# Kernel tuning notes

Hardware: AMD Instinct MI355X
Metric: run time of the kernel (lower is better)

The kernel has to match this reference:

```python
import jax, jax.numpy as jnp
import numpy as np

N_NODES = 50000
N_EDGES = 800000
N_GRAPHS = 512
HIDDEN = 256
NODE_FEAT = 9
LAYERS = 4


def setup_inputs() -> dict:
    key = jax.random.key(0)
    ks = jax.random.split(key, 9)
    x = jax.random.normal(ks[0], (N_NODES, NODE_FEAT), dtype=jnp.float32)
    edge_index = jax.random.randint(ks[1], (2, N_EDGES), 0, N_NODES, dtype=jnp.int64)
    batch = jnp.sort(jax.random.randint(ks[2], (N_NODES,), 0, N_GRAPHS, dtype=jnp.int64))
    embed_W = jax.random.normal(ks[3], (NODE_FEAT, HIDDEN), dtype=jnp.float32) * (1.0 / np.sqrt(NODE_FEAT))
    embed_b = jnp.zeros((HIDDEN,), dtype=jnp.float32)
    conv_W = jax.random.normal(ks[4], (LAYERS, HIDDEN, HIDDEN), dtype=jnp.float32) * (1.0 / np.sqrt(HIDDEN))
    conv_b = jnp.zeros((LAYERS, HIDDEN), dtype=jnp.float32)
    out_W = jax.random.normal(ks[5], (HIDDEN, 1), dtype=jnp.float32) * (1.0 / np.sqrt(HIDDEN))
    out_b = jnp.zeros((1,), dtype=jnp.float32)
    return {"x": x, "edge_index": edge_index, "batch": batch,
            "embed_W": embed_W, "embed_b": embed_b,
            "conv_W": conv_W, "conv_b": conv_b,
            "out_W": out_W, "out_b": out_b}


def reference(x, edge_index, batch, embed_W, embed_b, conv_W, conv_b, out_W, out_b):
    n = x.shape[0]
    src, dst = edge_index[0], edge_index[1]
    # GCN symmetric normalization with self-loops: deg includes the self-loop (+1)
    deg = jax.ops.segment_sum(jnp.ones(src.shape[0], x.dtype), dst, num_segments=n) + 1.0
    dinv = jax.lax.rsqrt(deg)                       # [N]
    norm_e = dinv[src] * dinv[dst]                  # [E] edge coefficient
    self_coef = (dinv * dinv)[:, None]              # [N,1] self-loop coefficient

    h = jax.nn.relu(x @ embed_W + embed_b)          # [N,H]
    for l in range(conv_W.shape[0]):
        hw = h @ conv_W[l]                          # [N,H] transform first
        msg = hw[src] * norm_e[:, None]             # [E,H] gather + scale
        agg = jax.ops.segment_sum(msg, dst, num_segments=n)  # scatter-add
        agg = agg + hw * self_coef                  # self-loop contribution
        h = jax.nn.relu(agg + conv_b[l])

    # global mean pool over graph ids
    sums = jax.ops.segment_sum(h, batch, num_segments=N_GRAPHS)           # [G,H]
    cnt = jax.ops.segment_sum(jnp.ones(n, h.dtype), batch, num_segments=N_GRAPHS)
    pooled = sums / jnp.maximum(cnt, 1.0)[:, None]
    return pooled @ out_W + out_b                   # [G,1]
```

## Files before the change

kernel.cpp:

```cpp
#include <hip/hip_runtime.h>

#define N_NODES 50000
#define N_EDGES 800000
#define N_GRAPHS 512
#define HIDDEN 256
#define NODE_FEAT 9
#define LAYERS 4
#define BUCKET 64

typedef float floatx4 __attribute__((ext_vector_type(4)));
typedef short short8 __attribute__((ext_vector_type(8)));

__device__ __forceinline__ float bf2f(unsigned u) {
    unsigned v = u << 16;
    float f;
    __builtin_memcpy(&f, &v, 4);
    return f;
}
__device__ __forceinline__ unsigned short f2bf(float f) {
    unsigned v;
    __builtin_memcpy(&v, &f, 4);
    v += 0x7FFFu + ((v >> 16) & 1u);
    return (unsigned short)(v >> 16);
}

__global__ void fillb_kernel(const int* __restrict__ src, const int* __restrict__ dst,
                             int* __restrict__ cnt, int* __restrict__ col_src, int E) {
    int e = blockIdx.x * blockDim.x + threadIdx.x;
    if (e < E) {
        int d = dst[e];
        int pos = atomicAdd(&cnt[d], 1);
        if (pos < BUCKET) col_src[d * BUCKET + pos] = src[e];
    }
}

__global__ void dinv_kernel(const int* __restrict__ cnt, float* __restrict__ dinv, int N) {
    int i = blockIdx.x * blockDim.x + threadIdx.x;
    if (i < N) dinv[i] = rsqrtf((float)(cnt[i] + 1));
}

__global__ void findstart_kernel(const int* __restrict__ batch, int* __restrict__ gstart) {
    int g = blockIdx.x * blockDim.x + threadIdx.x;
    if (g > N_GRAPHS) return;
    if (g == N_GRAPHS) { gstart[g] = N_NODES; return; }
    int lo = 0, hi = N_NODES;
    while (lo < hi) {
        int mid = (lo + hi) >> 1;
        if (batch[mid] < g) lo = mid + 1; else hi = mid;
    }
    gstart[g] = lo;
}

__global__ __launch_bounds__(256) void packW_kernel(const float* __restrict__ W,
                                                    unsigned short* __restrict__ Wsw) {
    int idx = blockIdx.x * 256 + threadIdx.x;
    int lane = idx & 63;
    int ct   = (idx >> 6) & 15;
    int ks   = (idx >> 10) & 7;
    int l    = idx >> 13;
    int n = ct * 16 + (lane & 15);
    int kbase = ks * 32 + (lane >> 4) * 8;
    const float* Wl = W + (size_t)l * HIDDEN * HIDDEN;
    alignas(16) unsigned short tmp[8];
    #pragma unroll
    for (int j = 0; j < 8; j++)
        tmp[j] = f2bf(Wl[(size_t)(kbase + j) * HIDDEN + n]);
    *(uint4*)&Wsw[(size_t)idx * 8] = *(const uint4*)tmp;
}

__global__ __launch_bounds__(256) void embed_kernel(const float* __restrict__ x,
                                                    const float* __restrict__ W,
                                                    const float* __restrict__ b,
                                                    unsigned short* __restrict__ h) {
    int n = blockIdx.x;
    int c = threadIdx.x;
    float acc = b[c];
    #pragma unroll
    for (int k = 0; k < NODE_FEAT; k++)
        acc += x[n * NODE_FEAT + k] * W[k * HIDDEN + c];
    h[(size_t)n * HIDDEN + c] = f2bf(fmaxf(acc, 0.0f));
}

__global__ __launch_bounds__(256, 2) void gemm_mfma(const unsigned short* __restrict__ hin,
                                                    const unsigned short* __restrict__ Wsw,
                                                    unsigned short* __restrict__ hwout, int N) {
    __shared__ unsigned short As[64][264];
    int t = threadIdx.x;
    int wv = t >> 6, lane = t & 63, quad = lane >> 4, l15 = lane & 15;
    int n0 = blockIdx.x * 64;
    const uint4* h4 = (const uint4*)hin;

    uint4 av[8];
    #pragma unroll
    for (int i = 0; i < 8; i++) {
        int j = t + i * 256;
        int r = j >> 5;
        int c = j & 31;
        int n = n0 + r;
        av[i] = make_uint4(0u, 0u, 0u, 0u);
        if (n < N) av[i] = h4[(size_t)n * 32 + c];
    }
    const short8* Wl = (const short8*)Wsw;
    short8 bq[3][4];
    #pragma unroll
    for (int p = 0; p < 2; p++)
        #pragma unroll
        for (int ci = 0; ci < 4; ci++)
            bq[p][ci] = Wl[(size_t)(p * 16 + wv * 4 + ci) * 64 + lane];
    #pragma unroll
    for (int i = 0; i < 8; i++) {
        int j = t + i * 256;
        int r = j >> 5;
        int c = j & 31;
        *(uint4*)&As[r][c * 8] = av[i];
    }
    __syncthreads();

    floatx4 acc[4][4];
    #pragma unroll
    for (int i = 0; i < 4; i++)
        #pragma unroll
        for (int j = 0; j < 4; j++)
            acc[i][j] = (floatx4){0.f, 0.f, 0.f, 0.f};

    #pragma unroll
    for (int ks = 0; ks < 8; ks++) {
        if (ks < 6) {
            #pragma unroll
            for (int ci = 0; ci < 4; ci++)
                bq[(ks + 2) % 3][ci] = Wl[(size_t)((ks + 2) * 16 + wv * 4 + ci) * 64 + lane];
        }
        short8 a[4];
        #pragma unroll
        for (int rt = 0; rt < 4; rt++)
            a[rt] = *(const short8*)&As[rt * 16 + l15][ks * 32 + quad * 8];
        #pragma unroll
        for (int rt = 0; rt < 4; rt++)
            #pragma unroll
            for (int ci = 0; ci < 4; ci++)
                acc[rt][ci] = __builtin_amdgcn_mfma_f32_16x16x32_bf16(a[rt], bq[ks % 3][ci], acc[rt][ci], 0, 0, 0);
    }

    __syncthreads();
    #pragma unroll
    for (int rt = 0; rt < 4; rt++) {
        #pragma unroll
        for (int ci = 0; ci < 4; ci++) {
            int col = (wv * 4 + ci) * 16 + l15;
            int rowb = rt * 16 + quad * 4;
            #pragma unroll
            for (int reg = 0; reg < 4; reg++)
                As[rowb + reg][col] = f2bf(acc[rt][ci][reg]);
        }
    }
    __syncthreads();
    #pragma unroll
    for (int i = 0; i < 8; i++) {
        int j = t + i * 256;
        int r = j >> 5;
        int c = j & 31;
        int n = n0 + r;
        if (n < N)
            *(uint4*)&hwout[(size_t)n * HIDDEN + c * 8] = *(const uint4*)&As[r][c * 8];
    }
}

__global__ __launch_bounds__(256) void agg_kernel(const unsigned short* __restrict__ hw,
                                                  const int* __restrict__ cnt,
                                                  const int* __restrict__ col_src,
                                                  const float* __restrict__ dinv,
                                                  const float* __restrict__ bias,
                                                  unsigned short* __restrict__ hout) {
    __shared__ uint2 sEdge[4][64];
    int wv = threadIdx.x >> 6, lane = threadIdx.x & 63;
    int n = blockIdx.x * 4 + wv;
    if (n >= N_NODES) return;
    float dn = dinv[n];
    int deg = cnt[n]; if (deg > BUCKET) deg = BUCKET;

    uint2 s2 = ((const uint2*)(hw + (size_t)n * HIDDEN))[lane];
    float4 b4 = *(const float4*)&bias[4 * lane];
    float selfc = dn * dn;
    float a0 = bf2f(s2.x & 0xFFFFu) * selfc + b4.x;
    float a1 = bf2f(s2.x >> 16)     * selfc + b4.y;
    float a2 = bf2f(s2.y & 0xFFFFu) * selfc + b4.z;
    float a3 = bf2f(s2.y >> 16)     * selfc + b4.w;

    if (lane < deg) {
        int s = col_src[n * BUCKET + lane];
        float nr = dinv[s] * dn;
        unsigned nrb;
        __builtin_memcpy(&nrb, &nr, 4);
        sEdge[wv][lane] = make_uint2((unsigned)s, nrb);
    }
    for (int i = 0; i < deg; i++) {
        uint2 p = sEdge[wv][i];
        float nr;
        __builtin_memcpy(&nr, &p.y, 4);
        uint2 u = ((const uint2*)(hw + (size_t)p.x * HIDDEN))[lane];
        a0 += nr * bf2f(u.x & 0xFFFFu);
        a1 += nr * bf2f(u.x >> 16);
        a2 += nr * bf2f(u.y & 0xFFFFu);
        a3 += nr * bf2f(u.y >> 16);
    }
    unsigned p0 = (unsigned)f2bf(fmaxf(a0, 0.0f)) | ((unsigned)f2bf(fmaxf(a1, 0.0f)) << 16);
    unsigned p1 = (unsigned)f2bf(fmaxf(a2, 0.0f)) | ((unsigned)f2bf(fmaxf(a3, 0.0f)) << 16);
    ((uint2*)(hout + (size_t)n * HIDDEN))[lane] = make_uint2(p0, p1);
}

__global__ __launch_bounds__(256) void pool2_kernel(const unsigned short* __restrict__ h,
                                                    const int* __restrict__ gstart,
                                                    const float* __restrict__ outW,
                                                    const float* __restrict__ outb,
                                                    float* __restrict__ out) {
    __shared__ float sred[4];
    int g = blockIdx.x;
    int t = threadIdx.x;
    int s = gstart[g], e = gstart[g + 1];
    int half = t >> 7;
    int tc = t & 127;
    float w0 = outW[2 * tc], w1 = outW[2 * tc + 1];
    float acc = 0.0f;
    for (int n = s + half; n < e; n += 2) {
        unsigned u = *(const unsigned*)&h[(size_t)n * HIDDEN + 2 * tc];
        acc += w0 * bf2f(u & 0xFFFFu) + w1 * bf2f(u >> 16);
    }
    #pragma unroll
    for (int off = 32; off > 0; off >>= 1) acc += __shfl_down(acc, off, 64);
    if ((t & 63) == 0) sred[t >> 6] = acc;
    __syncthreads();
    if (t == 0) {
        float tot = sred[0] + sred[1] + sred[2] + sred[3];
        float cntf = (float)(e - s);
        out[g] = tot / fmaxf(cntf, 1.0f) + outb[0];
    }
}

extern "C" void kernel_launch(void* const* d_in, const int* in_sizes, int n_in,
                              void* d_out, int out_size, void* d_ws, size_t ws_size,
                              hipStream_t stream) {
    const float* x     = (const float*)d_in[0];
    const int*   edge  = (const int*)d_in[1];
    const int*   src   = edge;
    const int*   dst   = edge + N_EDGES;
    const int*   batch = (const int*)d_in[2];
    const float* embW  = (const float*)d_in[3];
    const float* embb  = (const float*)d_in[4];
    const float* convW = (const float*)d_in[5];
    const float* convb = (const float*)d_in[6];
    const float* outW  = (const float*)d_in[7];
    const float* outb  = (const float*)d_in[8];
    float* out = (float*)d_out;

    char* ws = (char*)d_ws;
    size_t off = 0;
    auto take = [&](size_t bytes) { char* p = ws + off; off += (bytes + 255) & ~(size_t)255; return p; };
    int*   cnt     = (int*)  take((size_t)N_NODES * 4);
    int*   col_src = (int*)  take((size_t)N_NODES * BUCKET * 4);
    float* dinv    = (float*)take((size_t)N_NODES * 4);
    int*   gstart  = (int*)  take((size_t)(N_GRAPHS + 1) * 4);
    unsigned short* Wsw = (unsigned short*)take((size_t)LAYERS * 8 * 16 * 64 * 8 * 2);
    unsigned short* h0  = (unsigned short*)take((size_t)N_NODES * HIDDEN * 2);
    unsigned short* h1  = (unsigned short*)take((size_t)N_NODES * HIDDEN * 2);

    hipMemsetAsync(cnt, 0, (size_t)N_NODES * 4, stream);

    fillb_kernel<<<(N_EDGES + 255) / 256, 256, 0, stream>>>(src, dst, cnt, col_src, N_EDGES);
    dinv_kernel<<<(N_NODES + 255) / 256, 256, 0, stream>>>(cnt, dinv, N_NODES);
    findstart_kernel<<<3, 256, 0, stream>>>(batch, gstart);

    packW_kernel<<<128, 256, 0, stream>>>(convW, Wsw);
    embed_kernel<<<N_NODES, 256, 0, stream>>>(x, embW, embb, h0);

    unsigned short* ha = h0;
    unsigned short* hb = h1;
    for (int l = 0; l < LAYERS; l++) {
        gemm_mfma<<<(N_NODES + 63) / 64, 256, 0, stream>>>(ha, Wsw + (size_t)l * 65536, hb, N_NODES);
        agg_kernel<<<(N_NODES + 3) / 4, 256, 0, stream>>>(hb, cnt, col_src, dinv, convb + (size_t)l * HIDDEN, ha);
    }

    pool2_kernel<<<N_GRAPHS, 256, 0, stream>>>(ha, gstart, outW, outb, out);
}
```

Baseline: 466.2 us.

## Fuse embedding into first GEMM and aggregation into following layer GEMM

Merges the embedding into the first layer's MFMA GEMM, and fuses each layer's neighbour aggregation with the next layer's GEMM. Each block aggregates 64 rows straight into shared memory before multiplying. This removes the round trip of the hidden activations through global memory and cuts kernel launches from ten to six. In exchange, each block of 64 rows aggregates two nodes per wave in sequence, so there is less parallelism for the gather phase and load balance is worse. Occupancy is also bounded by the larger shared-memory footprint.

```diff
diff --git a/kernel.cpp b/kernel.cpp
--- a/kernel.cpp
+++ b/kernel.cpp
@@ -68,38 +68,11 @@
     *(uint4*)&Wsw[(size_t)idx * 8] = *(const uint4*)tmp;
 }
 
-__global__ __launch_bounds__(256) void embed_kernel(const float* __restrict__ x,
-                                                    const float* __restrict__ W,
-                                                    const float* __restrict__ b,
-                                                    unsigned short* __restrict__ h) {
-    int n = blockIdx.x;
-    int c = threadIdx.x;
-    float acc = b[c];
-    #pragma unroll
-    for (int k = 0; k < NODE_FEAT; k++)
-        acc += x[n * NODE_FEAT + k] * W[k * HIDDEN + c];
-    h[(size_t)n * HIDDEN + c] = f2bf(fmaxf(acc, 0.0f));
-}
-
-__global__ __launch_bounds__(256, 2) void gemm_mfma(const unsigned short* __restrict__ hin,
-                                                    const unsigned short* __restrict__ Wsw,
-                                                    unsigned short* __restrict__ hwout, int N) {
-    __shared__ unsigned short As[64][264];
-    int t = threadIdx.x;
+__device__ __forceinline__ void gemm_phase(unsigned short (*As)[264],
+                                           const unsigned short* __restrict__ Wsw,
+                                           unsigned short* __restrict__ hwout,
+                                           int n0, int N, int t) {
     int wv = t >> 6, lane = t & 63, quad = lane >> 4, l15 = lane & 15;
-    int n0 = blockIdx.x * 64;
-    const uint4* h4 = (const uint4*)hin;
-
-    uint4 av[8];
-    #pragma unroll
-    for (int i = 0; i < 8; i++) {
-        int j = t + i * 256;
-        int r = j >> 5;
-        int c = j & 31;
-        int n = n0 + r;
-        av[i] = make_uint4(0u, 0u, 0u, 0u);
-        if (n < N) av[i] = h4[(size_t)n * 32 + c];
-    }
     const short8* Wl = (const short8*)Wsw;
     short8 bq[3][4];
     #pragma unroll
@@ -107,13 +80,6 @@
         #pragma unroll
         for (int ci = 0; ci < 4; ci++)
             bq[p][ci] = Wl[(size_t)(p * 16 + wv * 4 + ci) * 64 + lane];
-    #pragma unroll
-    for (int i = 0; i < 8; i++) {
-        int j = t + i * 256;
-        int r = j >> 5;
-        int c = j & 31;
-        *(uint4*)&As[r][c * 8] = av[i];
-    }
     __syncthreads();
 
     floatx4 acc[4][4];
@@ -163,6 +129,120 @@
         if (n < N)
             *(uint4*)&hwout[(size_t)n * HIDDEN + c * 8] = *(const uint4*)&As[r][c * 8];
     }
+}
+
+__global__ __launch_bounds__(256, 2) void embed_gemm(const float* __restrict__ x,
+                                                     const float* __restrict__ embW,
+                                                     const float* __restrict__ embb,
+                                                     const unsigned short* __restrict__ Wsw,
+                                                     unsigned short* __restrict__ hwout, int N) {
+    __shared__ unsigned short As[64][264];
+    __shared__ float xs[64][10];
+    __shared__ float Ws[NODE_FEAT][HIDDEN];
+    int t = threadIdx.x;
+    int n0 = blockIdx.x * 64;
+    for (int i = t; i < NODE_FEAT * HIDDEN; i += 256)
+        ((float*)Ws)[i] = embW[i];
+    for (int i = t; i < 64 * NODE_FEAT; i += 256) {
+        int r = i / NODE_FEAT, k = i % NODE_FEAT;
+        int n = n0 + r;
+        xs[r][k] = (n < N) ? x[(size_t)n * NODE_FEAT + k] : 0.0f;
+    }
+    __syncthreads();
+    float bc = embb[t];
+    for (int r = 0; r < 64; r++) {
+        float acc = bc;
+        #pragma unroll
+        for (int k = 0; k < NODE_FEAT; k++)
+            acc += xs[r][k] * Ws[k][t];
+        As[r][t] = f2bf(fmaxf(acc, 0.0f));
+    }
+    gemm_phase(As, Wsw, hwout, n0, N, t);
+}
+
+__global__ __launch_bounds__(256, 2) void agg_gemm(const unsigned short* __restrict__ hwprev,
+                                                   const int* __restrict__ cnt,
+                                                   const int* __restrict__ col_src,
+                                                   const float* __restrict__ dinv,
+                                                   const float* __restrict__ bias,
+                                                   const unsigned short* __restrict__ Wsw,
+                                                   unsigned short* __restrict__ hwout, int N) {
+    __shared__ unsigned short As[64][264];
+    __shared__ uint2 sEdge[4][2][64];
+    int t = threadIdx.x;
+    int wv = t >> 6, lane = t & 63;
+    int n0 = blockIdx.x * 64;
+    float4 b4 = *(const float4*)&bias[4 * lane];
+
+    for (int i = 0; i < 8; i++) {
+        int rA = wv * 16 + i, rB = rA + 8;
+        int nA = n0 + rA, nB = n0 + rB;
+        bool vA = nA < N, vB = nB < N;
+        float dnA = 0.f, dnB = 0.f;
+        int degA = 0, degB = 0;
+        float a0 = 0.f, a1 = 0.f, a2 = 0.f, a3 = 0.f;
+        float c0 = 0.f, c1 = 0.f, c2 = 0.f, c3 = 0.f;
+        if (vA) {
+            dnA = dinv[nA];
+            degA = cnt[nA]; if (degA > BUCKET) degA = BUCKET;
+            uint2 s2 = ((const uint2*)(hwprev + (size_t)nA * HIDDEN))[lane];
+            float sc = dnA * dnA;
+            a0 = bf2f(s2.x & 0xFFFFu) * sc + b4.x;
+            a1 = bf2f(s2.x >> 16)     * sc + b4.y;
+            a2 = bf2f(s2.y & 0xFFFFu) * sc + b4.z;
+            a3 = bf2f(s2.y >> 16)     * sc + b4.w;
+            if (lane < degA) {
+                int s = col_src[nA * BUCKET + lane];
+                float nr = dinv[s] * dnA;
+                unsigned nrb; __builtin_memcpy(&nrb, &nr, 4);
+                sEdge[wv][0][lane] = make_uint2((unsigned)s, nrb);
+            }
+        }
+        if (vB) {
+            dnB = dinv[nB];
+            degB = cnt[nB]; if (degB > BUCKET) degB = BUCKET;
+            uint2 s2 = ((const uint2*)(hwprev + (size_t)nB * HIDDEN))[lane];
+            float sc = dnB * dnB;
+            c0 = bf2f(s2.x & 0xFFFFu) * sc + b4.x;
+            c1 = bf2f(s2.x >> 16)     * sc + b4.y;
+            c2 = bf2f(s2.y & 0xFFFFu) * sc + b4.z;
+            c3 = bf2f(s2.y >> 16)     * sc + b4.w;
+            if (lane < degB) {
+                int s = col_src[nB * BUCKET + lane];
+                float nr = dinv[s] * dnB;
+                unsigned nrb; __builtin_memcpy(&nrb, &nr, 4);
+                sEdge[wv][1][lane] = make_uint2((unsigned)s, nrb);
+            }
+        }
+        int dm = degA > degB ? degA : degB;
+        for (int k = 0; k < dm; k++) {
+            if (k < degA) {
+                uint2 p = sEdge[wv][0][k];
+                float nr; __builtin_memcpy(&nr, &p.y, 4);
+                uint2 u = ((const uint2*)(hwprev + (size_t)p.x * HIDDEN))[lane];
+                a0 += nr * bf2f(u.x & 0xFFFFu);
+                a1 += nr * bf2f(u.x >> 16);
+                a2 += nr * bf2f(u.y & 0xFFFFu);
+                a3 += nr * bf2f(u.y >> 16);
+            }
+            if (k < degB) {
+                uint2 p = sEdge[wv][1][k];
+                float nr; __builtin_memcpy(&nr, &p.y, 4);
+                uint2 u = ((const uint2*)(hwprev + (size_t)p.x * HIDDEN))[lane];
+                c0 += nr * bf2f(u.x & 0xFFFFu);
+                c1 += nr * bf2f(u.x >> 16);
+                c2 += nr * bf2f(u.y & 0xFFFFu);
+                c3 += nr * bf2f(u.y >> 16);
+            }
+        }
+        unsigned pA0 = (unsigned)f2bf(fmaxf(a0, 0.f)) | ((unsigned)f2bf(fmaxf(a1, 0.f)) << 16);
+        unsigned pA1 = (unsigned)f2bf(fmaxf(a2, 0.f)) | ((unsigned)f2bf(fmaxf(a3, 0.f)) << 16);
+        unsigned pB0 = (unsigned)f2bf(fmaxf(c0, 0.f)) | ((unsigned)f2bf(fmaxf(c1, 0.f)) << 16);
+        unsigned pB1 = (unsigned)f2bf(fmaxf(c2, 0.f)) | ((unsigned)f2bf(fmaxf(c3, 0.f)) << 16);
+        *(uint2*)&As[rA][4 * lane] = vA ? make_uint2(pA0, pA1) : make_uint2(0u, 0u);
+        *(uint2*)&As[rB][4 * lane] = vB ? make_uint2(pB0, pB1) : make_uint2(0u, 0u);
+    }
+    gemm_phase(As, Wsw, hwout, n0, N, t);
 }
 
 __global__ __launch_bounds__(256) void agg_kernel(const unsigned short* __restrict__ hw,
@@ -268,16 +348,13 @@
     fillb_kernel<<<(N_EDGES + 255) / 256, 256, 0, stream>>>(src, dst, cnt, col_src, N_EDGES);
     dinv_kernel<<<(N_NODES + 255) / 256, 256, 0, stream>>>(cnt, dinv, N_NODES);
     findstart_kernel<<<3, 256, 0, stream>>>(batch, gstart);
-
     packW_kernel<<<128, 256, 0, stream>>>(convW, Wsw);
-    embed_kernel<<<N_NODES, 256, 0, stream>>>(x, embW, embb, h0);
-
-    unsigned short* ha = h0;
-    unsigned short* hb = h1;
-    for (int l = 0; l < LAYERS; l++) {
-        gemm_mfma<<<(N_NODES + 63) / 64, 256, 0, stream>>>(ha, Wsw + (size_t)l * 65536, hb, N_NODES);
-        agg_kernel<<<(N_NODES + 3) / 4, 256, 0, stream>>>(hb, cnt, col_src, dinv, convb + (size_t)l * HIDDEN, ha);
-    }
-
-    pool2_kernel<<<N_GRAPHS, 256, 0, stream>>>(ha, gstart, outW, outb, out);
-}
+
+    int nb = (N_NODES + 63) / 64;
+    embed_gemm<<<nb, 256, 0, stream>>>(x, embW, embb, Wsw, h1, N_NODES);
+    agg_gemm<<<nb, 256, 0, stream>>>(h1, cnt, col_src, dinv, convb + 0 * HIDDEN, Wsw + 1 * 65536, h0, N_NODES);
+    agg_gemm<<<nb, 256, 0, stream>>>(h0, cnt, col_src, dinv, convb + 1 * HIDDEN, Wsw + 2 * 65536, h1, N_NODES);
+    agg_gemm<<<nb, 256, 0, stream>>>(h1, cnt, col_src, dinv, convb + 2 * HIDDEN, Wsw + 3 * 65536, h0, N_NODES);
+    agg_kernel<<<(N_NODES + 3) / 4, 256, 0, stream>>>(h0, cnt, col_src, dinv, convb + 3 * HIDDEN, h1);
+    pool2_kernel<<<N_GRAPHS, 256, 0, stream>>>(h1, gstart, outW, outb, out);
+}
```

Result: slower. 883.4 us (+89.5%).

## Split aggregation across feature slices with eight nodes per wavefront

Applied to the files above, without the earlier changes.

Replaces the one-wavefront-per-node aggregation with a sliced kernel: each block handles one 32-column feature slice for 64 nodes, so each wavefront serves 8 nodes with 8 lanes each. The aim is to keep each block's gathered working set to one slice of the feature table, improving L2/MALL locality, and to spread per-node degree imbalance across lanes. The cost is that every wavefront now makes 64-byte gathers instead of full 512-byte rows, and edge indices and dinv are reloaded once per slice (8x redundant index traffic). Per-node loop lengths also diverge within a wavefront.

```diff
diff --git a/kernel.cpp b/kernel.cpp
--- a/kernel.cpp
+++ b/kernel.cpp
@@ -7,6 +7,7 @@
 #define NODE_FEAT 9
 #define LAYERS 4
 #define BUCKET 64
+#define SLICES 8
 
 typedef float floatx4 __attribute__((ext_vector_type(4)));
 typedef short short8 __attribute__((ext_vector_type(8)));
@@ -165,47 +166,48 @@
     }
 }
 
-__global__ __launch_bounds__(256) void agg_kernel(const unsigned short* __restrict__ hw,
-                                                  const int* __restrict__ cnt,
-                                                  const int* __restrict__ col_src,
-                                                  const float* __restrict__ dinv,
-                                                  const float* __restrict__ bias,
-                                                  unsigned short* __restrict__ hout) {
-    __shared__ uint2 sEdge[4][64];
-    int wv = threadIdx.x >> 6, lane = threadIdx.x & 63;
-    int n = blockIdx.x * 4 + wv;
-    if (n >= N_NODES) return;
-    float dn = dinv[n];
-    int deg = cnt[n]; if (deg > BUCKET) deg = BUCKET;
-
-    uint2 s2 = ((const uint2*)(hw + (size_t)n * HIDDEN))[lane];
-    float4 b4 = *(const float4*)&bias[4 * lane];
-    float selfc = dn * dn;
-    float a0 = bf2f(s2.x & 0xFFFFu) * selfc + b4.x;
-    float a1 = bf2f(s2.x >> 16)     * selfc + b4.y;
-    float a2 = bf2f(s2.y & 0xFFFFu) * selfc + b4.z;
-    float a3 = bf2f(s2.y >> 16)     * selfc + b4.w;
-
-    if (lane < deg) {
-        int s = col_src[n * BUCKET + lane];
-        float nr = dinv[s] * dn;
-        unsigned nrb;
-        __builtin_memcpy(&nrb, &nr, 4);
-        sEdge[wv][lane] = make_uint2((unsigned)s, nrb);
-    }
-    for (int i = 0; i < deg; i++) {
-        uint2 p = sEdge[wv][i];
-        float nr;
-        __builtin_memcpy(&nr, &p.y, 4);
-        uint2 u = ((const uint2*)(hw + (size_t)p.x * HIDDEN))[lane];
-        a0 += nr * bf2f(u.x & 0xFFFFu);
-        a1 += nr * bf2f(u.x >> 16);
-        a2 += nr * bf2f(u.y & 0xFFFFu);
-        a3 += nr * bf2f(u.y >> 16);
-    }
-    unsigned p0 = (unsigned)f2bf(fmaxf(a0, 0.0f)) | ((unsigned)f2bf(fmaxf(a1, 0.0f)) << 16);
-    unsigned p1 = (unsigned)f2bf(fmaxf(a2, 0.0f)) | ((unsigned)f2bf(fmaxf(a3, 0.0f)) << 16);
-    ((uint2*)(hout + (size_t)n * HIDDEN))[lane] = make_uint2(p0, p1);
+__global__ __launch_bounds__(256) void agg_slice(const unsigned short* __restrict__ hw,
+                                                 const int* __restrict__ cnt,
+                                                 const int* __restrict__ col_src,
+                                                 const float* __restrict__ dinv,
+                                                 const float* __restrict__ bias,
+                                                 unsigned short* __restrict__ hout) {
+    int slice = blockIdx.x & (SLICES - 1);
+    int chunk = blockIdx.x / SLICES;
+    int t = threadIdx.x;
+    int wv = t >> 6, lane = t & 63;
+    int sub = lane >> 3, sl = lane & 7;
+    const uint2* hw2 = (const uint2*)hw;
+    int ci = slice * 8 + sl;
+    float4 bA = *(const float4*)&bias[slice * 32 + sl * 4];
+
+    #pragma unroll
+    for (int it = 0; it < 2; it++) {
+        int n = chunk * 64 + it * 32 + wv * 8 + sub;
+        if (n < N_NODES) {
+            float dn = dinv[n];
+            int deg = cnt[n]; if (deg > BUCKET) deg = BUCKET;
+            uint2 su = hw2[(size_t)n * 64 + ci];
+            float sc = dn * dn;
+            float a0 = bf2f(su.x & 0xFFFFu) * sc + bA.x;
+            float a1 = bf2f(su.x >> 16)     * sc + bA.y;
+            float a2 = bf2f(su.y & 0xFFFFu) * sc + bA.z;
+            float a3 = bf2f(su.y >> 16)     * sc + bA.w;
+            const int* bucket = col_src + (size_t)n * BUCKET;
+            for (int k = 0; k < deg; k++) {
+                int s = bucket[k];
+                float nr = dinv[s] * dn;
+                uint2 u = hw2[(size_t)s * 64 + ci];
+                a0 += nr * bf2f(u.x & 0xFFFFu);
+                a1 += nr * bf2f(u.x >> 16);
+                a2 += nr * bf2f(u.y & 0xFFFFu);
+                a3 += nr * bf2f(u.y >> 16);
+            }
+            unsigned p0 = (unsigned)f2bf(fmaxf(a0, 0.f)) | ((unsigned)f2bf(fmaxf(a1, 0.f)) << 16);
+            unsigned p1 = (unsigned)f2bf(fmaxf(a2, 0.f)) | ((unsigned)f2bf(fmaxf(a3, 0.f)) << 16);
+            ((uint2*)hout)[(size_t)n * 64 + ci] = make_uint2(p0, p1);
+        }
+    }
 }
 
 __global__ __launch_bounds__(256) void pool2_kernel(const unsigned short* __restrict__ h,
@@ -268,15 +270,15 @@
     fillb_kernel<<<(N_EDGES + 255) / 256, 256, 0, stream>>>(src, dst, cnt, col_src, N_EDGES);
     dinv_kernel<<<(N_NODES + 255) / 256, 256, 0, stream>>>(cnt, dinv, N_NODES);
     findstart_kernel<<<3, 256, 0, stream>>>(batch, gstart);
-
     packW_kernel<<<128, 256, 0, stream>>>(convW, Wsw);
     embed_kernel<<<N_NODES, 256, 0, stream>>>(x, embW, embb, h0);
 
+    int agg_grid = ((N_NODES + 63) / 64) * SLICES;
     unsigned short* ha = h0;
     unsigned short* hb = h1;
     for (int l = 0; l < LAYERS; l++) {
         gemm_mfma<<<(N_NODES + 63) / 64, 256, 0, stream>>>(ha, Wsw + (size_t)l * 65536, hb, N_NODES);
-        agg_kernel<<<(N_NODES + 3) / 4, 256, 0, stream>>>(hb, cnt, col_src, dinv, convb + (size_t)l * HIDDEN, ha);
+        agg_slice<<<agg_grid, 256, 0, stream>>>(hb, cnt, col_src, dinv, convb + (size_t)l * HIDDEN, ha);
     }
 
     pool2_kernel<<<N_GRAPHS, 256, 0, stream>>>(ha, gstart, outW, outb, out);
```

After: 906.9 us. +94.5%, slower.
